# Kernel optimization log

Measured on AMD Instinct MI355X. Metric: run time of the kernel, lower is better.

The kernel has to match this reference:

```python
import jax, jax.numpy as jnp
import numpy as np
from jax import lax

DN = ('NCHW', 'OIHW', 'NCHW')

def conv(x, w, b, stride):
    y = lax.conv_general_dilated(x, w, window_strides=(stride, stride),
                                 padding='VALID', dimension_numbers=DN)
    return y + b[None, :, None, None]

def setup_inputs() -> dict:
    key = jax.random.key(0)
    ks = jax.random.split(key, 7)
    B = 4096
    def he(k, shape, fan_in):
        return jax.random.normal(k, shape, jnp.float32) * np.sqrt(2.0 / fan_in)
    return {
        'x':  jax.random.normal(ks[0], (B, 3, 48, 64), jnp.float32),
        'w1': he(ks[1], (32, 3, 8, 8), 3 * 8 * 8),
        'b1': jnp.zeros((32,), jnp.float32),
        'w2': he(ks[2], (64, 32, 3, 3), 32 * 3 * 3),
        'b2': jnp.zeros((64,), jnp.float32),
        'w3': he(ks[3], (64, 64, 3, 3), 64 * 3 * 3),
        'b3': jnp.zeros((64,), jnp.float32),
        'w4': he(ks[4], (512, 960), 960),
        'b4': jnp.zeros((512,), jnp.float32),
        'w5': he(ks[5], (2, 512), 512),
        'b5': jnp.zeros((2,), jnp.float32),
    }

def reference(x, w1, b1, w2, b2, w3, b3, w4, b4, w5, b5):
    # conv1 (k8 s4): [B,3,48,64] -> [B,32,11,15]
    x1 = conv(x, w1, b1, 4)
    # side reduction (torch code does this on CPU with python loops):
    # sum over batch and channel dims of pre-ReLU activation, divided by 32
    ave1 = jnp.sum(x1, axis=(0, 1)) / 32.0          # [11,15]
    x2 = jax.nn.relu(x1)
    # conv2 (k3 s2): -> [B,64,5,7]
    x3 = conv(x2, w2, b2, 2)
    ave2 = jnp.sum(x3, axis=(0, 1)) / 64.0          # [5,7]
    x4 = jax.nn.relu(x3)
    # conv3 (k3 s1): -> [B,64,3,5]
    x5 = conv(x4, w3, b3, 1)
    ave3 = jnp.sum(x5, axis=(0, 1)) / 64.0          # [3,5]
    x6 = jax.nn.relu(x5)
    # fc head: flatten (C,H,W order, matching torch) -> 960 -> 512 -> 2
    h = x6.reshape(x6.shape[0], -1)                 # [B,960]
    h = jax.nn.relu(h @ w4.T + b4)
    out = h @ w5.T + b5                             # [B,2]
    return out, ave1, ave2, ave3
```

## Files before the change

### kernel.cpp

```cpp
#include <hip/hip_runtime.h>
#include <hip/hip_bf16.h>

#define BATCH 4096

typedef __attribute__((ext_vector_type(8))) short short8;
typedef __attribute__((ext_vector_type(4))) short short4_t;
typedef __attribute__((ext_vector_type(4))) float f32x4;

#define MFMA_BF16 __builtin_amdgcn_mfma_f32_16x16x32_bf16

__device__ __forceinline__ float frelu(float v) { return v > 0.f ? v : 0.f; }
__device__ __forceinline__ unsigned short f2bf(float f) {
    return __builtin_bit_cast(unsigned short, __float2bfloat16(f));
}

__global__ __launch_bounds__(256) void prep_kernel(const float* __restrict__ w1, const float* __restrict__ w2,
                                                   const float* __restrict__ w3, const float* __restrict__ w4,
                                                   const float* __restrict__ b5,
                                                   unsigned short* __restrict__ w1p, unsigned short* __restrict__ w2p,
                                                   unsigned short* __restrict__ w3p, unsigned short* __restrict__ w4p,
                                                   float* __restrict__ out) {
    int idx = blockIdx.x * 256 + threadIdx.x;
    if (idx < 6144) {
        w1p[idx] = f2bf(w1[idx]);
    } else if (idx < 24576) {
        int j = idx - 6144;
        int oc = j / 288, k = j % 288;
        int khw = k / 32, ic = k % 32;
        w2p[j] = f2bf(w2[oc * 288 + ic * 9 + khw]);
    } else if (idx < 61440) {
        int j = idx - 24576;
        int oc = j / 576, k = j % 576;
        int khw = k / 64, ic = k % 64;
        w3p[j] = f2bf(w3[oc * 576 + ic * 9 + khw]);
    } else if (idx < 552960) {
        int j = idx - 61440;
        int n = j / 960, k = j % 960;
        int pos = k / 64, oc = k % 64;
        w4p[j] = f2bf(w4[n * 960 + oc * 15 + pos]);
    } else if (idx < 561152) {
        int j = idx - 552960;
        out[j] = b5[j & 1];
    } else if (idx < 561367) {
        out[8192 + (idx - 561152)] = 0.f;
    }
}

__global__ __launch_bounds__(256, 8) void fused_convs(const float* __restrict__ x,
                                                      const unsigned short* __restrict__ w1p, const float* __restrict__ b1,
                                                      const unsigned short* __restrict__ w2p, const float* __restrict__ b2,
                                                      const unsigned short* __restrict__ w3p, const float* __restrict__ b3,
                                                      unsigned short* __restrict__ x6, float* __restrict__ redbuf) {
    constexpr int RS = 68;
    __shared__ __align__(16) unsigned short ub[3 * 48 * RS];
    __shared__ float red[215];
    unsigned short* x2l = ub;
    unsigned short* x4l = ub + 5952;
    unsigned short* x6l = ub + 8480;

    const int img = blockIdx.x;
    const int tid = threadIdx.x;
    const int wave = tid >> 6, lane = tid & 63;
    const int col = lane & 15, quad = lane >> 4;

    if (tid < 215) red[tid] = 0.f;

    {
        const float4* xs = (const float4*)(x + (size_t)img * 9216);
        #pragma unroll
        for (int i = 0; i < 9; ++i) {
            const int idx = tid + i * 256;
            float4 v = xs[idx];
            const int fo = idx * 4;
            const int r = fo >> 6, cf = fo & 63;
            short4_t s;
            s[0] = (short)f2bf(v.x); s[1] = (short)f2bf(v.y);
            s[2] = (short)f2bf(v.z); s[3] = (short)f2bf(v.w);
            *(short4_t*)(ub + r * RS + cf) = s;
        }
    }
    const float bias0 = b1[col], bias1 = b1[col + 16];
    __syncthreads();

    f32x4 c1a[3][2] = {};
    const unsigned short* w1b0 = w1p + (size_t)col * 192 + quad * 8;
    const unsigned short* w1b1 = w1b0 + 16 * 192;
    #pragma unroll
    for (int ti = 0; ti < 3; ++ti) {
        const int t = wave + ti * 4;
        if (t >= 11) break;
        const int posA = t * 16 + col;
        const int pm = posA < 165 ? posA : 164;
        const int oh = pm / 15, ow = pm % 15;
        #pragma unroll
        for (int c = 0; c < 6; ++c) {
            const int ic = c >> 1;
            const int kh = (c & 1) * 4 + quad;
            const unsigned short* ap = ub + (ic * 48 + oh * 4 + kh) * RS + ow * 4;
            short8 af;
            *(short4_t*)&af       = *(const short4_t*)ap;
            *((short4_t*)&af + 1) = *(const short4_t*)(ap + 4);
            short8 B0 = *(const short8*)(w1b0 + c * 32);
            short8 B1 = *(const short8*)(w1b1 + c * 32);
            c1a[ti][0] = MFMA_BF16(af, B0, c1a[ti][0], 0, 0, 0);
            c1a[ti][1] = MFMA_BF16(af, B1, c1a[ti][1], 0, 0, 0);
        }
    }
    __syncthreads();

    #pragma unroll
    for (int ti = 0; ti < 3; ++ti) {
        const int t = wave + ti * 4;
        if (t >= 11) break;
        #pragma unroll
        for (int r = 0; r < 4; ++r) {
            const int pr = t * 16 + quad * 4 + r;
            float v0 = c1a[ti][0][r] + bias0;
            float v1 = c1a[ti][1][r] + bias1;
            float s = v0 + v1;
            s += __shfl_xor(s, 1); s += __shfl_xor(s, 2);
            s += __shfl_xor(s, 4); s += __shfl_xor(s, 8);
            if (pr < 165) {
                if (col == 0) atomicAdd(&red[pr], s);
                x2l[pr * 36 + col]      = f2bf(frelu(v0));
                x2l[pr * 36 + col + 16] = f2bf(frelu(v1));
            }
        }
    }
    __syncthreads();

    {
        const int oc2 = wave * 16 + col;
        const unsigned short* w2b = w2p + (size_t)oc2 * 288 + quad * 8;
        int aoff[3];
        #pragma unroll
        for (int mt = 0; mt < 3; ++mt) {
            int p = mt * 16 + col; p = p < 35 ? p : 34;
            aoff[mt] = ((p / 7) * 30 + (p % 7) * 2) * 36 + quad * 8;
        }
        f32x4 a2[3] = {};
        #pragma unroll
        for (int c = 0; c < 9; ++c) {
            short8 Bc = *(const short8*)(w2b + c * 32);
            const int koff = ((c / 3) * 15 + (c % 3)) * 36;
            #pragma unroll
            for (int mt = 0; mt < 3; ++mt) {
                const unsigned short* ap = x2l + aoff[mt] + koff;
                short8 af;
                *(short4_t*)&af       = *(const short4_t*)ap;
                *((short4_t*)&af + 1) = *(const short4_t*)(ap + 4);
                a2[mt] = MFMA_BF16(af, Bc, a2[mt], 0, 0, 0);
            }
        }
        const float bv2 = b2[oc2];
        #pragma unroll
        for (int mt = 0; mt < 3; ++mt) {
            #pragma unroll
            for (int r = 0; r < 4; ++r) {
                const int pr = mt * 16 + quad * 4 + r;
                float v = a2[mt][r] + bv2;
                float s = v;
                s += __shfl_xor(s, 1); s += __shfl_xor(s, 2);
                s += __shfl_xor(s, 4); s += __shfl_xor(s, 8);
                if (pr < 35) {
                    x4l[pr * 72 + oc2] = f2bf(frelu(v));
                    if (col == 0) atomicAdd(&red[165 + pr], s);
                }
            }
        }
    }
    __syncthreads();

    {
        const int oc3 = wave * 16 + col;
        const unsigned short* w3b = w3p + (size_t)oc3 * 576 + quad * 8;
        int p = col < 15 ? col : 14;
        const int abase = ((p / 5) * 7 + (p % 5)) * 72;
        f32x4 aA = {}, aB = {};
        #pragma unroll
        for (int cc = 0; cc < 9; ++cc) {
            const int kh = cc / 3, kw = cc % 3;
            const unsigned short* bp = x4l + abase + (kh * 7 + kw) * 72 + quad * 8;
            short8 af0 = *(const short8*)bp;
            short8 af1 = *(const short8*)(bp + 32);
            short8 B0 = *(const short8*)(w3b + (2 * cc) * 32);
            short8 B1 = *(const short8*)(w3b + (2 * cc + 1) * 32);
            aA = MFMA_BF16(af0, B0, aA, 0, 0, 0);
            aB = MFMA_BF16(af1, B1, aB, 0, 0, 0);
        }
        f32x4 a3 = aA + aB;
        const float bv3 = b3[oc3];
        #pragma unroll
        for (int r = 0; r < 4; ++r) {
            const int pr = quad * 4 + r;
            float v = a3[r] + bv3;
            float s = v;
            s += __shfl_xor(s, 1); s += __shfl_xor(s, 2);
            s += __shfl_xor(s, 4); s += __shfl_xor(s, 8);
            if (pr < 15) {
                x6l[pr * 64 + oc3] = f2bf(frelu(v));
                if (col == 0) atomicAdd(&red[200 + pr], s);
            }
        }
    }
    __syncthreads();

    if (tid < 120) ((float4*)(x6 + (size_t)img * 960))[tid] = ((const float4*)x6l)[tid];
    if (tid < 215) redbuf[(size_t)img * 216 + tid] = red[tid];
}

__global__ __launch_bounds__(256) void reduce_aves(const float* __restrict__ redbuf, float* __restrict__ out) {
    const int row = blockIdx.x;
    float s = 0.f;
    for (int i = threadIdx.x; i < 4096; i += 256) s += redbuf[(size_t)i * 216 + row];
    s += __shfl_down(s, 32); s += __shfl_down(s, 16); s += __shfl_down(s, 8);
    s += __shfl_down(s, 4);  s += __shfl_down(s, 2);  s += __shfl_down(s, 1);
    __shared__ float wsum[4];
    if ((threadIdx.x & 63) == 0) wsum[threadIdx.x >> 6] = s;
    __syncthreads();
    if (threadIdx.x == 0)
        out[8192 + row] = (wsum[0] + wsum[1] + wsum[2] + wsum[3]) * (row < 165 ? 0.03125f : 0.015625f);
}

__global__ __launch_bounds__(256) void fc45_mfma(const unsigned short* __restrict__ x6,
                                                 const unsigned short* __restrict__ w4p, const float* __restrict__ b4,
                                                 const float* __restrict__ w5, float* __restrict__ out) {
    __shared__ float outl[32][2];
    const int tid = threadIdx.x;
    const int wave = tid >> 6, lane = tid & 63;
    const int col = lane & 15, quad = lane >> 4;
    if (tid < 64) outl[tid >> 1][tid & 1] = 0.f;
    const int m0 = blockIdx.x * 32;
    const int oc = blockIdx.y * 64 + wave * 16 + col;

    const unsigned short* brow  = w4p + (size_t)oc * 960 + quad * 8;
    const unsigned short* arow0 = x6 + (size_t)(m0 + col) * 960 + quad * 8;
    const unsigned short* arow1 = arow0 + 16 * 960;
    f32x4 acc0 = {}, acc1 = {};
    __syncthreads();
    #pragma unroll 6
    for (int c = 0; c < 30; ++c) {
        short8 Bf = *(const short8*)(brow + c * 32);
        short8 a0 = *(const short8*)(arow0 + c * 32);
        short8 a1 = *(const short8*)(arow1 + c * 32);
        acc0 = MFMA_BF16(a0, Bf, acc0, 0, 0, 0);
        acc1 = MFMA_BF16(a1, Bf, acc1, 0, 0, 0);
    }
    const float bb = b4[oc], u0 = w5[oc], u1 = w5[512 + oc];
    #pragma unroll
    for (int mi = 0; mi < 2; ++mi) {
        const f32x4 acc = mi ? acc1 : acc0;
        #pragma unroll
        for (int r = 0; r < 4; ++r) {
            float h = frelu(acc[r] + bb);
            float l0 = h * u0, l1 = h * u1;
            l0 += __shfl_xor(l0, 1); l0 += __shfl_xor(l0, 2); l0 += __shfl_xor(l0, 4); l0 += __shfl_xor(l0, 8);
            l1 += __shfl_xor(l1, 1); l1 += __shfl_xor(l1, 2); l1 += __shfl_xor(l1, 4); l1 += __shfl_xor(l1, 8);
            if (col == 0) {
                atomicAdd(&outl[mi * 16 + quad * 4 + r][0], l0);
                atomicAdd(&outl[mi * 16 + quad * 4 + r][1], l1);
            }
        }
    }
    __syncthreads();
    if (tid < 64) atomicAdd(&out[(m0 + (tid >> 1)) * 2 + (tid & 1)], outl[tid >> 1][tid & 1]);
}

extern "C" void kernel_launch(void* const* d_in, const int* in_sizes, int n_in,
                              void* d_out, int out_size, void* d_ws, size_t ws_size,
                              hipStream_t stream) {
    const float* x  = (const float*)d_in[0];
    const float* w1 = (const float*)d_in[1];
    const float* b1 = (const float*)d_in[2];
    const float* w2 = (const float*)d_in[3];
    const float* b2 = (const float*)d_in[4];
    const float* w3 = (const float*)d_in[5];
    const float* b3 = (const float*)d_in[6];
    const float* w4 = (const float*)d_in[7];
    const float* b4 = (const float*)d_in[8];
    const float* w5 = (const float*)d_in[9];
    const float* b5 = (const float*)d_in[10];
    float* out = (float*)d_out;

    unsigned short* ws = (unsigned short*)d_ws;
    unsigned short* x6  = ws;
    unsigned short* w1p = ws + 3932160;
    unsigned short* w2p = ws + 3938304;
    unsigned short* w3p = ws + 3956736;
    unsigned short* w4p = ws + 3993600;
    float* redbuf = (float*)((char*)d_ws + 8970240);

    prep_kernel<<<2193, 256, 0, stream>>>(w1, w2, w3, w4, b5, w1p, w2p, w3p, w4p, out);
    fused_convs<<<BATCH, 256, 0, stream>>>(x, w1p, b1, w2p, b2, w3p, b3, x6, redbuf);
    reduce_aves<<<215, 256, 0, stream>>>(redbuf, out);
    fc45_mfma<<<dim3(128, 8), 256, 0, stream>>>(x6, w4p, b4, w5, out);
}
```

Measured before the change: 349.2 us.

## Process four images per block with register prefetch of next image input

The fused conv kernel now loops over four images per block and launches a quarter as many blocks. While the current image is converted to bf16 and computed, the next image's fp32 input is prefetched into registers. Barriers become LDS-only waits (lgkmcnt + s_barrier) so the global prefetch loads can stay in flight across them. x4l and x6l move out of the ub alias into their own buffers, and launch bounds drop to 4 blocks per CU. The aim is to hide input-load latency and amortise block setup, at the cost of 36 extra registers per thread for the prefetch and less parallelism from fewer blocks.

```diff
diff --git a/kernel.cpp b/kernel.cpp
--- a/kernel.cpp
+++ b/kernel.cpp
@@ -8,6 +8,8 @@
 typedef __attribute__((ext_vector_type(4))) float f32x4;
 
 #define MFMA_BF16 __builtin_amdgcn_mfma_f32_16x16x32_bf16
+
+#define LBAR() asm volatile("s_waitcnt lgkmcnt(0)\n\ts_barrier" ::: "memory")
 
 __device__ __forceinline__ float frelu(float v) { return v > 0.f ? v : 0.f; }
 __device__ __forceinline__ unsigned short f2bf(float f) {
@@ -46,167 +48,183 @@
     }
 }
 
-__global__ __launch_bounds__(256, 8) void fused_convs(const float* __restrict__ x,
+__global__ __launch_bounds__(256, 4) void fused_convs(const float* __restrict__ x,
                                                       const unsigned short* __restrict__ w1p, const float* __restrict__ b1,
                                                       const unsigned short* __restrict__ w2p, const float* __restrict__ b2,
                                                       const unsigned short* __restrict__ w3p, const float* __restrict__ b3,
                                                       unsigned short* __restrict__ x6, float* __restrict__ redbuf) {
     constexpr int RS = 68;
     __shared__ __align__(16) unsigned short ub[3 * 48 * RS];
+    __shared__ __align__(16) unsigned short x4l[35 * 72];
+    __shared__ __align__(16) unsigned short x6l[15 * 64];
     __shared__ float red[215];
     unsigned short* x2l = ub;
-    unsigned short* x4l = ub + 5952;
-    unsigned short* x6l = ub + 8480;
-
-    const int img = blockIdx.x;
+
     const int tid = threadIdx.x;
     const int wave = tid >> 6, lane = tid & 63;
     const int col = lane & 15, quad = lane >> 4;
-
-    if (tid < 215) red[tid] = 0.f;
-
+    const int img0 = blockIdx.x * 4;
+
+    const float bias0 = b1[col], bias1 = b1[col + 16];
+
+    float4 pf[9];
     {
-        const float4* xs = (const float4*)(x + (size_t)img * 9216);
+        const float4* xs = (const float4*)(x + (size_t)img0 * 9216);
+        #pragma unroll
+        for (int i = 0; i < 9; ++i) pf[i] = xs[tid + i * 256];
+    }
+
+    for (int it = 0; it < 4; ++it) {
+        const int img = img0 + it;
+
+        if (it > 0) {
+            if (tid < 120) ((float4*)(x6 + (size_t)(img - 1) * 960))[tid] = ((const float4*)x6l)[tid];
+            if (tid < 215) redbuf[(size_t)(img - 1) * 216 + tid] = red[tid];
+        }
+        if (tid < 215) red[tid] = 0.f;
         #pragma unroll
         for (int i = 0; i < 9; ++i) {
             const int idx = tid + i * 256;
-            float4 v = xs[idx];
-            const int fo = idx * 4;
-            const int r = fo >> 6, cf = fo & 63;
+            const int r = idx >> 4, cf = (idx & 15) * 4;
+            float4 v = pf[i];
             short4_t s;
             s[0] = (short)f2bf(v.x); s[1] = (short)f2bf(v.y);
             s[2] = (short)f2bf(v.z); s[3] = (short)f2bf(v.w);
             *(short4_t*)(ub + r * RS + cf) = s;
         }
-    }
-    const float bias0 = b1[col], bias1 = b1[col + 16];
-    __syncthreads();
-
-    f32x4 c1a[3][2] = {};
-    const unsigned short* w1b0 = w1p + (size_t)col * 192 + quad * 8;
-    const unsigned short* w1b1 = w1b0 + 16 * 192;
-    #pragma unroll
-    for (int ti = 0; ti < 3; ++ti) {
-        const int t = wave + ti * 4;
-        if (t >= 11) break;
-        const int posA = t * 16 + col;
-        const int pm = posA < 165 ? posA : 164;
-        const int oh = pm / 15, ow = pm % 15;
-        #pragma unroll
-        for (int c = 0; c < 6; ++c) {
-            const int ic = c >> 1;
-            const int kh = (c & 1) * 4 + quad;
-            const unsigned short* ap = ub + (ic * 48 + oh * 4 + kh) * RS + ow * 4;
-            short8 af;
-            *(short4_t*)&af       = *(const short4_t*)ap;
-            *((short4_t*)&af + 1) = *(const short4_t*)(ap + 4);
-            short8 B0 = *(const short8*)(w1b0 + c * 32);
-            short8 B1 = *(const short8*)(w1b1 + c * 32);
-            c1a[ti][0] = MFMA_BF16(af, B0, c1a[ti][0], 0, 0, 0);
-            c1a[ti][1] = MFMA_BF16(af, B1, c1a[ti][1], 0, 0, 0);
-        }
-    }
-    __syncthreads();
-
-    #pragma unroll
-    for (int ti = 0; ti < 3; ++ti) {
-        const int t = wave + ti * 4;
-        if (t >= 11) break;
-        #pragma unroll
-        for (int r = 0; r < 4; ++r) {
-            const int pr = t * 16 + quad * 4 + r;
-            float v0 = c1a[ti][0][r] + bias0;
-            float v1 = c1a[ti][1][r] + bias1;
-            float s = v0 + v1;
-            s += __shfl_xor(s, 1); s += __shfl_xor(s, 2);
-            s += __shfl_xor(s, 4); s += __shfl_xor(s, 8);
-            if (pr < 165) {
-                if (col == 0) atomicAdd(&red[pr], s);
-                x2l[pr * 36 + col]      = f2bf(frelu(v0));
-                x2l[pr * 36 + col + 16] = f2bf(frelu(v1));
-            }
-        }
-    }
-    __syncthreads();
-
-    {
-        const int oc2 = wave * 16 + col;
-        const unsigned short* w2b = w2p + (size_t)oc2 * 288 + quad * 8;
-        int aoff[3];
-        #pragma unroll
-        for (int mt = 0; mt < 3; ++mt) {
-            int p = mt * 16 + col; p = p < 35 ? p : 34;
-            aoff[mt] = ((p / 7) * 30 + (p % 7) * 2) * 36 + quad * 8;
-        }
-        f32x4 a2[3] = {};
-        #pragma unroll
-        for (int c = 0; c < 9; ++c) {
-            short8 Bc = *(const short8*)(w2b + c * 32);
-            const int koff = ((c / 3) * 15 + (c % 3)) * 36;
-            #pragma unroll
-            for (int mt = 0; mt < 3; ++mt) {
-                const unsigned short* ap = x2l + aoff[mt] + koff;
+        if (it < 3) {
+            const float4* xs = (const float4*)(x + (size_t)(img + 1) * 9216);
+            #pragma unroll
+            for (int i = 0; i < 9; ++i) pf[i] = xs[tid + i * 256];
+        }
+        LBAR();
+
+        f32x4 c1a[3][2] = {};
+        const unsigned short* w1b0 = w1p + (size_t)col * 192 + quad * 8;
+        const unsigned short* w1b1 = w1b0 + 16 * 192;
+        #pragma unroll
+        for (int ti = 0; ti < 3; ++ti) {
+            const int t = wave + ti * 4;
+            if (t >= 11) break;
+            const int posA = t * 16 + col;
+            const int pm = posA < 165 ? posA : 164;
+            const int oh = pm / 15, ow = pm % 15;
+            #pragma unroll
+            for (int c = 0; c < 6; ++c) {
+                const int ic = c >> 1;
+                const int kh = (c & 1) * 4 + quad;
+                const unsigned short* ap = ub + (ic * 48 + oh * 4 + kh) * RS + ow * 4;
                 short8 af;
                 *(short4_t*)&af       = *(const short4_t*)ap;
                 *((short4_t*)&af + 1) = *(const short4_t*)(ap + 4);
-                a2[mt] = MFMA_BF16(af, Bc, a2[mt], 0, 0, 0);
-            }
-        }
-        const float bv2 = b2[oc2];
-        #pragma unroll
-        for (int mt = 0; mt < 3; ++mt) {
+                short8 B0 = *(const short8*)(w1b0 + c * 32);
+                short8 B1 = *(const short8*)(w1b1 + c * 32);
+                c1a[ti][0] = MFMA_BF16(af, B0, c1a[ti][0], 0, 0, 0);
+                c1a[ti][1] = MFMA_BF16(af, B1, c1a[ti][1], 0, 0, 0);
+            }
+        }
+        LBAR();
+
+        #pragma unroll
+        for (int ti = 0; ti < 3; ++ti) {
+            const int t = wave + ti * 4;
+            if (t >= 11) break;
             #pragma unroll
             for (int r = 0; r < 4; ++r) {
-                const int pr = mt * 16 + quad * 4 + r;
-                float v = a2[mt][r] + bv2;
+                const int pr = t * 16 + quad * 4 + r;
+                float v0 = c1a[ti][0][r] + bias0;
+                float v1 = c1a[ti][1][r] + bias1;
+                float s = v0 + v1;
+                s += __shfl_xor(s, 1); s += __shfl_xor(s, 2);
+                s += __shfl_xor(s, 4); s += __shfl_xor(s, 8);
+                if (pr < 165) {
+                    if (col == 0) atomicAdd(&red[pr], s);
+                    x2l[pr * 36 + col]      = f2bf(frelu(v0));
+                    x2l[pr * 36 + col + 16] = f2bf(frelu(v1));
+                }
+            }
+        }
+        LBAR();
+
+        {
+            const int oc2 = wave * 16 + col;
+            const unsigned short* w2b = w2p + (size_t)oc2 * 288 + quad * 8;
+            int aoff[3];
+            #pragma unroll
+            for (int mt = 0; mt < 3; ++mt) {
+                int p = mt * 16 + col; p = p < 35 ? p : 34;
+                aoff[mt] = ((p / 7) * 30 + (p % 7) * 2) * 36 + quad * 8;
+            }
+            f32x4 a2[3] = {};
+            #pragma unroll
+            for (int c = 0; c < 9; ++c) {
+                short8 Bc = *(const short8*)(w2b + c * 32);
+                const int koff = ((c / 3) * 15 + (c % 3)) * 36;
+                #pragma unroll
+                for (int mt = 0; mt < 3; ++mt) {
+                    const unsigned short* ap = x2l + aoff[mt] + koff;
+                    short8 af;
+                    *(short4_t*)&af       = *(const short4_t*)ap;
+                    *((short4_t*)&af + 1) = *(const short4_t*)(ap + 4);
+                    a2[mt] = MFMA_BF16(af, Bc, a2[mt], 0, 0, 0);
+                }
+            }
+            const float bv2 = b2[oc2];
+            #pragma unroll
+            for (int mt = 0; mt < 3; ++mt) {
+                #pragma unroll
+                for (int r = 0; r < 4; ++r) {
+                    const int pr = mt * 16 + quad * 4 + r;
+                    float v = a2[mt][r] + bv2;
+                    float s = v;
+                    s += __shfl_xor(s, 1); s += __shfl_xor(s, 2);
+                    s += __shfl_xor(s, 4); s += __shfl_xor(s, 8);
+                    if (pr < 35) {
+                        x4l[pr * 72 + oc2] = f2bf(frelu(v));
+                        if (col == 0) atomicAdd(&red[165 + pr], s);
+                    }
+                }
+            }
+        }
+        LBAR();
+
+        {
+            const int oc3 = wave * 16 + col;
+            const unsigned short* w3b = w3p + (size_t)oc3 * 576 + quad * 8;
+            int p = col < 15 ? col : 14;
+            const int abase = ((p / 5) * 7 + (p % 5)) * 72;
+            f32x4 aA = {}, aB = {};
+            #pragma unroll
+            for (int cc = 0; cc < 9; ++cc) {
+                const int kh = cc / 3, kw = cc % 3;
+                const unsigned short* bp = x4l + abase + (kh * 7 + kw) * 72 + quad * 8;
+                short8 af0 = *(const short8*)bp;
+                short8 af1 = *(const short8*)(bp + 32);
+                short8 B0 = *(const short8*)(w3b + (2 * cc) * 32);
+                short8 B1 = *(const short8*)(w3b + (2 * cc + 1) * 32);
+                aA = MFMA_BF16(af0, B0, aA, 0, 0, 0);
+                aB = MFMA_BF16(af1, B1, aB, 0, 0, 0);
+            }
+            f32x4 a3 = aA + aB;
+            const float bv3 = b3[oc3];
+            #pragma unroll
+            for (int r = 0; r < 4; ++r) {
+                const int pr = quad * 4 + r;
+                float v = a3[r] + bv3;
                 float s = v;
                 s += __shfl_xor(s, 1); s += __shfl_xor(s, 2);
                 s += __shfl_xor(s, 4); s += __shfl_xor(s, 8);
-                if (pr < 35) {
-                    x4l[pr * 72 + oc2] = f2bf(frelu(v));
-                    if (col == 0) atomicAdd(&red[165 + pr], s);
+                if (pr < 15) {
+                    x6l[pr * 64 + oc3] = f2bf(frelu(v));
+                    if (col == 0) atomicAdd(&red[200 + pr], s);
                 }
             }
         }
-    }
-    __syncthreads();
-
-    {
-        const int oc3 = wave * 16 + col;
-        const unsigned short* w3b = w3p + (size_t)oc3 * 576 + quad * 8;
-        int p = col < 15 ? col : 14;
-        const int abase = ((p / 5) * 7 + (p % 5)) * 72;
-        f32x4 aA = {}, aB = {};
-        #pragma unroll
-        for (int cc = 0; cc < 9; ++cc) {
-            const int kh = cc / 3, kw = cc % 3;
-            const unsigned short* bp = x4l + abase + (kh * 7 + kw) * 72 + quad * 8;
-            short8 af0 = *(const short8*)bp;
-            short8 af1 = *(const short8*)(bp + 32);
-            short8 B0 = *(const short8*)(w3b + (2 * cc) * 32);
-            short8 B1 = *(const short8*)(w3b + (2 * cc + 1) * 32);
-            aA = MFMA_BF16(af0, B0, aA, 0, 0, 0);
-            aB = MFMA_BF16(af1, B1, aB, 0, 0, 0);
-        }
-        f32x4 a3 = aA + aB;
-        const float bv3 = b3[oc3];
-        #pragma unroll
-        for (int r = 0; r < 4; ++r) {
-            const int pr = quad * 4 + r;
-            float v = a3[r] + bv3;
-            float s = v;
-            s += __shfl_xor(s, 1); s += __shfl_xor(s, 2);
-            s += __shfl_xor(s, 4); s += __shfl_xor(s, 8);
-            if (pr < 15) {
-                x6l[pr * 64 + oc3] = f2bf(frelu(v));
-                if (col == 0) atomicAdd(&red[200 + pr], s);
-            }
-        }
-    }
-    __syncthreads();
-
-    if (tid < 120) ((float4*)(x6 + (size_t)img * 960))[tid] = ((const float4*)x6l)[tid];
-    if (tid < 215) redbuf[(size_t)img * 216 + tid] = red[tid];
+        LBAR();
+    }
+
+    if (tid < 120) ((float4*)(x6 + (size_t)(img0 + 3) * 960))[tid] = ((const float4*)x6l)[tid];
+    if (tid < 215) redbuf[(size_t)(img0 + 3) * 216 + tid] = red[tid];
 }
 
 __global__ __launch_bounds__(256) void reduce_aves(const float* __restrict__ redbuf, float* __restrict__ out) {
@@ -291,7 +309,7 @@
     float* redbuf = (float*)((char*)d_ws + 8970240);
 
     prep_kernel<<<2193, 256, 0, stream>>>(w1, w2, w3, w4, b5, w1p, w2p, w3p, w4p, out);
-    fused_convs<<<BATCH, 256, 0, stream>>>(x, w1p, b1, w2p, b2, w3p, b3, x6, redbuf);
+    fused_convs<<<1024, 256, 0, stream>>>(x, w1p, b1, w2p, b2, w3p, b3, x6, redbuf);
     reduce_aves<<<215, 256, 0, stream>>>(redbuf, out);
     fc45_mfma<<<dim3(128, 8), 256, 0, stream>>>(x6, w4p, b4, w5, out);
 }
```

Result: slower. 401.7 us (+15.0%).

## Process one image per wave in fused conv kernel, dropping block barriers

Applied to the files above, without the earlier changes.

Changes the work split in the fused conv kernel from one image per 256-thread block to one image per 64-lane wave, with four images per block. Each wave keeps its own LDS slice and computes every output channel tile itself. Block-wide __syncthreads become lgkmcnt waits, and LDS atomics for the side reductions become direct global stores. Per-wave register use rises sharply (11x2 conv1 accumulators, 12 conv2 accumulators, preloaded weights) and launch_bounds drops to 2 blocks per CU, so occupancy and latency hiding may suffer. Relying on s_waitcnt alone for intra-wave LDS ordering also carries correctness risk.

```diff
diff --git a/kernel.cpp b/kernel.cpp
--- a/kernel.cpp
+++ b/kernel.cpp
@@ -8,6 +8,8 @@
 typedef __attribute__((ext_vector_type(4))) float f32x4;
 
 #define MFMA_BF16 __builtin_amdgcn_mfma_f32_16x16x32_bf16
+
+#define WWAIT() asm volatile("s_waitcnt lgkmcnt(0)" ::: "memory")
 
 __device__ __forceinline__ float frelu(float v) { return v > 0.f ? v : 0.f; }
 __device__ __forceinline__ unsigned short f2bf(float f) {
@@ -46,49 +48,52 @@
     }
 }
 
-__global__ __launch_bounds__(256, 8) void fused_convs(const float* __restrict__ x,
+__global__ __launch_bounds__(256, 2) void fused_convs(const float* __restrict__ x,
                                                       const unsigned short* __restrict__ w1p, const float* __restrict__ b1,
                                                       const unsigned short* __restrict__ w2p, const float* __restrict__ b2,
                                                       const unsigned short* __restrict__ w3p, const float* __restrict__ b3,
                                                       unsigned short* __restrict__ x6, float* __restrict__ redbuf) {
-    constexpr int RS = 68;
-    __shared__ __align__(16) unsigned short ub[3 * 48 * RS];
-    __shared__ float red[215];
-    unsigned short* x2l = ub;
-    unsigned short* x4l = ub + 5952;
-    unsigned short* x6l = ub + 8480;
-
-    const int img = blockIdx.x;
+    __shared__ __align__(16) unsigned short S[4][9792];
     const int tid = threadIdx.x;
     const int wave = tid >> 6, lane = tid & 63;
     const int col = lane & 15, quad = lane >> 4;
-
-    if (tid < 215) red[tid] = 0.f;
+    const int img = blockIdx.x * 4 + wave;
+
+    unsigned short* ub  = S[wave];
+    unsigned short* x2l = ub;
+    unsigned short* x4l = ub + 5952;
+    float* redrow = redbuf + (size_t)img * 216;
 
     {
         const float4* xs = (const float4*)(x + (size_t)img * 9216);
         #pragma unroll
-        for (int i = 0; i < 9; ++i) {
-            const int idx = tid + i * 256;
-            float4 v = xs[idx];
-            const int fo = idx * 4;
-            const int r = fo >> 6, cf = fo & 63;
-            short4_t s;
-            s[0] = (short)f2bf(v.x); s[1] = (short)f2bf(v.y);
-            s[2] = (short)f2bf(v.z); s[3] = (short)f2bf(v.w);
-            *(short4_t*)(ub + r * RS + cf) = s;
-        }
-    }
-    const float bias0 = b1[col], bias1 = b1[col + 16];
-    __syncthreads();
-
-    f32x4 c1a[3][2] = {};
-    const unsigned short* w1b0 = w1p + (size_t)col * 192 + quad * 8;
-    const unsigned short* w1b1 = w1b0 + 16 * 192;
+        for (int b = 0; b < 3; ++b) {
+            float4 t[12];
+            #pragma unroll
+            for (int i = 0; i < 12; ++i) t[i] = xs[lane + (b * 12 + i) * 64];
+            #pragma unroll
+            for (int i = 0; i < 12; ++i) {
+                const int idx = lane + (b * 12 + i) * 64;
+                const int r = idx >> 4, cf = (idx & 15) * 4;
+                short4_t s;
+                s[0] = (short)f2bf(t[i].x); s[1] = (short)f2bf(t[i].y);
+                s[2] = (short)f2bf(t[i].z); s[3] = (short)f2bf(t[i].w);
+                *(short4_t*)(ub + r * 68 + cf) = s;
+            }
+        }
+    }
+    WWAIT();
+
+    short8 Bf1[2][6];
     #pragma unroll
-    for (int ti = 0; ti < 3; ++ti) {
-        const int t = wave + ti * 4;
-        if (t >= 11) break;
+    for (int nt = 0; nt < 2; ++nt) {
+        const unsigned short* wb = w1p + (size_t)(nt * 16 + col) * 192 + quad * 8;
+        #pragma unroll
+        for (int c = 0; c < 6; ++c) Bf1[nt][c] = *(const short8*)(wb + c * 32);
+    }
+    f32x4 c1a[11][2] = {};
+    #pragma unroll
+    for (int t = 0; t < 11; ++t) {
         const int posA = t * 16 + col;
         const int pm = posA < 165 ? posA : 164;
         const int oh = pm / 15, ow = pm % 15;
@@ -96,117 +101,128 @@
         for (int c = 0; c < 6; ++c) {
             const int ic = c >> 1;
             const int kh = (c & 1) * 4 + quad;
-            const unsigned short* ap = ub + (ic * 48 + oh * 4 + kh) * RS + ow * 4;
+            const unsigned short* ap = ub + (ic * 48 + oh * 4 + kh) * 68 + ow * 4;
             short8 af;
             *(short4_t*)&af       = *(const short4_t*)ap;
             *((short4_t*)&af + 1) = *(const short4_t*)(ap + 4);
-            short8 B0 = *(const short8*)(w1b0 + c * 32);
-            short8 B1 = *(const short8*)(w1b1 + c * 32);
-            c1a[ti][0] = MFMA_BF16(af, B0, c1a[ti][0], 0, 0, 0);
-            c1a[ti][1] = MFMA_BF16(af, B1, c1a[ti][1], 0, 0, 0);
-        }
-    }
-    __syncthreads();
-
-    #pragma unroll
-    for (int ti = 0; ti < 3; ++ti) {
-        const int t = wave + ti * 4;
-        if (t >= 11) break;
-        #pragma unroll
-        for (int r = 0; r < 4; ++r) {
-            const int pr = t * 16 + quad * 4 + r;
-            float v0 = c1a[ti][0][r] + bias0;
-            float v1 = c1a[ti][1][r] + bias1;
-            float s = v0 + v1;
-            s += __shfl_xor(s, 1); s += __shfl_xor(s, 2);
-            s += __shfl_xor(s, 4); s += __shfl_xor(s, 8);
-            if (pr < 165) {
-                if (col == 0) atomicAdd(&red[pr], s);
-                x2l[pr * 36 + col]      = f2bf(frelu(v0));
-                x2l[pr * 36 + col + 16] = f2bf(frelu(v1));
-            }
-        }
-    }
-    __syncthreads();
+            c1a[t][0] = MFMA_BF16(af, Bf1[0][c], c1a[t][0], 0, 0, 0);
+            c1a[t][1] = MFMA_BF16(af, Bf1[1][c], c1a[t][1], 0, 0, 0);
+        }
+    }
+    WWAIT();
 
     {
-        const int oc2 = wave * 16 + col;
-        const unsigned short* w2b = w2p + (size_t)oc2 * 288 + quad * 8;
+        const float bias0 = b1[col], bias1 = b1[col + 16];
+        #pragma unroll
+        for (int t = 0; t < 11; ++t) {
+            #pragma unroll
+            for (int r = 0; r < 4; ++r) {
+                const int pr = t * 16 + quad * 4 + r;
+                float v0 = c1a[t][0][r] + bias0;
+                float v1 = c1a[t][1][r] + bias1;
+                float s = v0 + v1;
+                s += __shfl_xor(s, 1); s += __shfl_xor(s, 2);
+                s += __shfl_xor(s, 4); s += __shfl_xor(s, 8);
+                if (pr < 165) {
+                    x2l[pr * 36 + col]      = f2bf(frelu(v0));
+                    x2l[pr * 36 + col + 16] = f2bf(frelu(v1));
+                    if (col == 0) redrow[pr] = s;
+                }
+            }
+        }
+    }
+    WWAIT();
+
+    {
         int aoff[3];
         #pragma unroll
         for (int mt = 0; mt < 3; ++mt) {
             int p = mt * 16 + col; p = p < 35 ? p : 34;
             aoff[mt] = ((p / 7) * 30 + (p % 7) * 2) * 36 + quad * 8;
         }
-        f32x4 a2[3] = {};
+        f32x4 a2[3][4] = {};
         #pragma unroll
         for (int c = 0; c < 9; ++c) {
-            short8 Bc = *(const short8*)(w2b + c * 32);
             const int koff = ((c / 3) * 15 + (c % 3)) * 36;
+            short8 A[3];
             #pragma unroll
             for (int mt = 0; mt < 3; ++mt) {
                 const unsigned short* ap = x2l + aoff[mt] + koff;
-                short8 af;
-                *(short4_t*)&af       = *(const short4_t*)ap;
-                *((short4_t*)&af + 1) = *(const short4_t*)(ap + 4);
-                a2[mt] = MFMA_BF16(af, Bc, a2[mt], 0, 0, 0);
-            }
-        }
-        const float bv2 = b2[oc2];
+                *(short4_t*)&A[mt]       = *(const short4_t*)ap;
+                *((short4_t*)&A[mt] + 1) = *(const short4_t*)(ap + 4);
+            }
+            #pragma unroll
+            for (int nt = 0; nt < 4; ++nt) {
+                short8 Bc = *(const short8*)(w2p + (size_t)(nt * 16 + col) * 288 + c * 32 + quad * 8);
+                #pragma unroll
+                for (int mt = 0; mt < 3; ++mt)
+                    a2[mt][nt] = MFMA_BF16(A[mt], Bc, a2[mt][nt], 0, 0, 0);
+            }
+        }
+        float bv2[4];
+        #pragma unroll
+        for (int nt = 0; nt < 4; ++nt) bv2[nt] = b2[nt * 16 + col];
         #pragma unroll
         for (int mt = 0; mt < 3; ++mt) {
             #pragma unroll
             for (int r = 0; r < 4; ++r) {
                 const int pr = mt * 16 + quad * 4 + r;
-                float v = a2[mt][r] + bv2;
-                float s = v;
+                if (pr < 35) {
+                    float s = 0.f;
+                    #pragma unroll
+                    for (int nt = 0; nt < 4; ++nt) {
+                        float v = a2[mt][nt][r] + bv2[nt];
+                        s += v;
+                        x4l[pr * 72 + nt * 16 + col] = f2bf(frelu(v));
+                    }
+                    s += __shfl_xor(s, 1); s += __shfl_xor(s, 2);
+                    s += __shfl_xor(s, 4); s += __shfl_xor(s, 8);
+                    if (col == 0) redrow[165 + pr] = s;
+                }
+            }
+        }
+    }
+    WWAIT();
+
+    {
+        int p = col < 15 ? col : 14;
+        const int abase = ((p / 5) * 7 + (p % 5)) * 72;
+        f32x4 a3[4] = {};
+        #pragma unroll
+        for (int cc = 0; cc < 9; ++cc) {
+            const unsigned short* bp = x4l + abase + ((cc / 3) * 7 + (cc % 3)) * 72 + quad * 8;
+            short8 af0 = *(const short8*)bp;
+            short8 af1 = *(const short8*)(bp + 32);
+            #pragma unroll
+            for (int nt = 0; nt < 4; ++nt) {
+                const unsigned short* wb = w3p + (size_t)(nt * 16 + col) * 576 + quad * 8;
+                short8 B0 = *(const short8*)(wb + (2 * cc) * 32);
+                short8 B1 = *(const short8*)(wb + (2 * cc + 1) * 32);
+                a3[nt] = MFMA_BF16(af0, B0, a3[nt], 0, 0, 0);
+                a3[nt] = MFMA_BF16(af1, B1, a3[nt], 0, 0, 0);
+            }
+        }
+        float bv3[4];
+        #pragma unroll
+        for (int nt = 0; nt < 4; ++nt) bv3[nt] = b3[nt * 16 + col];
+        unsigned short* xout = x6 + (size_t)img * 960;
+        #pragma unroll
+        for (int r = 0; r < 4; ++r) {
+            const int pr = quad * 4 + r;
+            if (pr < 15) {
+                float s = 0.f;
+                #pragma unroll
+                for (int nt = 0; nt < 4; ++nt) {
+                    float v = a3[nt][r] + bv3[nt];
+                    s += v;
+                    xout[pr * 64 + nt * 16 + col] = f2bf(frelu(v));
+                }
                 s += __shfl_xor(s, 1); s += __shfl_xor(s, 2);
                 s += __shfl_xor(s, 4); s += __shfl_xor(s, 8);
-                if (pr < 35) {
-                    x4l[pr * 72 + oc2] = f2bf(frelu(v));
-                    if (col == 0) atomicAdd(&red[165 + pr], s);
-                }
-            }
-        }
-    }
-    __syncthreads();
-
-    {
-        const int oc3 = wave * 16 + col;
-        const unsigned short* w3b = w3p + (size_t)oc3 * 576 + quad * 8;
-        int p = col < 15 ? col : 14;
-        const int abase = ((p / 5) * 7 + (p % 5)) * 72;
-        f32x4 aA = {}, aB = {};
-        #pragma unroll
-        for (int cc = 0; cc < 9; ++cc) {
-            const int kh = cc / 3, kw = cc % 3;
-            const unsigned short* bp = x4l + abase + (kh * 7 + kw) * 72 + quad * 8;
-            short8 af0 = *(const short8*)bp;
-            short8 af1 = *(const short8*)(bp + 32);
-            short8 B0 = *(const short8*)(w3b + (2 * cc) * 32);
-            short8 B1 = *(const short8*)(w3b + (2 * cc + 1) * 32);
-            aA = MFMA_BF16(af0, B0, aA, 0, 0, 0);
-            aB = MFMA_BF16(af1, B1, aB, 0, 0, 0);
-        }
-        f32x4 a3 = aA + aB;
-        const float bv3 = b3[oc3];
-        #pragma unroll
-        for (int r = 0; r < 4; ++r) {
-            const int pr = quad * 4 + r;
-            float v = a3[r] + bv3;
-            float s = v;
-            s += __shfl_xor(s, 1); s += __shfl_xor(s, 2);
-            s += __shfl_xor(s, 4); s += __shfl_xor(s, 8);
-            if (pr < 15) {
-                x6l[pr * 64 + oc3] = f2bf(frelu(v));
-                if (col == 0) atomicAdd(&red[200 + pr], s);
-            }
-        }
-    }
-    __syncthreads();
-
-    if (tid < 120) ((float4*)(x6 + (size_t)img * 960))[tid] = ((const float4*)x6l)[tid];
-    if (tid < 215) redbuf[(size_t)img * 216 + tid] = red[tid];
+                if (col == 0) redrow[200 + pr] = s;
+            }
+        }
+    }
 }
 
 __global__ __launch_bounds__(256) void reduce_aves(const float* __restrict__ redbuf, float* __restrict__ out) {
@@ -291,7 +307,7 @@
     float* redbuf = (float*)((char*)d_ws + 8970240);
 
     prep_kernel<<<2193, 256, 0, stream>>>(w1, w2, w3, w4, b5, w1p, w2p, w3p, w4p, out);
-    fused_convs<<<BATCH, 256, 0, stream>>>(x, w1p, b1, w2p, b2, w3p, b3, x6, redbuf);
+    fused_convs<<<1024, 256, 0, stream>>>(x, w1p, b1, w2p, b2, w3p, b3, x6, redbuf);
     reduce_aves<<<215, 256, 0, stream>>>(redbuf, out);
     fc45_mfma<<<dim3(128, 8), 256, 0, stream>>>(x6, w4p, b4, w5, out);
 }
```

New measurement: 341.0 us. 1.02x faster.
